# Kernel optimization log

Measured on AMD Instinct MI355X. Metric: run time of the kernel, lower is better.

## Reference

```python
import jax, jax.numpy as jnp
import numpy as np
import math

D_MODEL = 1024
N_HEADS = 16
D_K = D_MODEL // N_HEADS
B, S = 4, 2048


def setup_inputs() -> dict:
    key = jax.random.key(0)
    ks = jax.random.split(key, 11)
    sc = 1.0 / math.sqrt(D_MODEL)
    inp = {
        'q': jax.random.normal(ks[0], (B, S, D_MODEL), jnp.float32),
        'k': jax.random.normal(ks[1], (B, S, D_MODEL), jnp.float32),
        'v': jax.random.normal(ks[2], (B, S, D_MODEL), jnp.float32),
        'mask': jnp.tril(jnp.ones((S, S), jnp.int32))[None, None],  # [1,1,S,S] causal
        'wq': jax.random.normal(ks[3], (D_MODEL, D_MODEL), jnp.float32) * sc,
        'bq': jnp.zeros((D_MODEL,), jnp.float32),
        'wk': jax.random.normal(ks[4], (D_MODEL, D_MODEL), jnp.float32) * sc,
        'bk': jnp.zeros((D_MODEL,), jnp.float32),
        'wv': jax.random.normal(ks[5], (D_MODEL, D_MODEL), jnp.float32) * sc,
        'bv': jnp.zeros((D_MODEL,), jnp.float32),
        'wo': jax.random.normal(ks[6], (D_MODEL, D_MODEL), jnp.float32) * sc,
        'bo': jnp.zeros((D_MODEL,), jnp.float32),
    }
    return inp


def reference(q, k, v, mask, wq, bq, wk, bk, wv, bv, wo, bo):
    b = q.shape[0]
    # projections: [B,S,D] -> [B,H,S,d_k]
    def split_heads(x):
        return x.reshape(b, -1, N_HEADS, D_K).transpose(0, 2, 1, 3)
    qh = split_heads(q @ wq + bq)
    kh = split_heads(k @ wk + bk)
    vh = split_heads(v @ wv + bv)
    # scores: [B,H,S,S]
    scores = jnp.einsum('bhqd,bhkd->bhqk', qh, kh) / math.sqrt(D_K)
    scores = jnp.where(mask == 0, jnp.float32(-1e9), scores)
    attn = jax.nn.softmax(scores, axis=-1)
    # dropout is identity in eval mode (deterministic reference)
    ctx = jnp.einsum('bhqk,bhkd->bhqd', attn, vh)
    ctx = ctx.transpose(0, 2, 1, 3).reshape(b, -1, D_MODEL)
    return ctx @ wo + bo
```

## Files before the change

### kernel.cpp

```cpp
#include <hip/hip_runtime.h>
#include <hip/hip_bf16.h>

#define D_MODEL 1024
#define N_HEADS 16
#define DK 64
#define SEQ 2048
#define BATCH 4

typedef __attribute__((ext_vector_type(4))) float   f32v4;
typedef __attribute__((ext_vector_type(16))) float  f32v16;
typedef __attribute__((ext_vector_type(8))) __bf16  bf16x8;
typedef __attribute__((ext_vector_type(8))) unsigned short u16v8;
typedef __attribute__((ext_vector_type(4))) unsigned short u16v4;
typedef __attribute__((ext_vector_type(4))) unsigned int   u32v4;

#define QSCALE 0.18033688011112042f

__device__ __forceinline__ int swz(int byte) {
    return byte ^ (((byte >> 7) & 7) << 4);
}

__device__ __forceinline__ unsigned short bfb(float f) {
    return __builtin_bit_cast(unsigned short, (__bf16)f);
}
__device__ __forceinline__ float bff(unsigned short u) {
    return (float)__builtin_bit_cast(__bf16, u);
}

__device__ __forceinline__ f32v4 mfma16(bf16x8 a, bf16x8 b, f32v4 c) {
    return __builtin_amdgcn_mfma_f32_16x16x32_bf16(a, b, c, 0, 0, 0);
}
__device__ __forceinline__ f32v16 mfma32(bf16x8 a, bf16x8 b, f32v16 c) {
    return __builtin_amdgcn_mfma_f32_32x32x16_bf16(a, b, c, 0, 0, 0);
}

#define GL2LDS16(gp, lp) \
    __builtin_amdgcn_global_load_lds((__attribute__((address_space(1))) const void*)(gp), \
                                     (__attribute__((address_space(3))) void*)(lp), 16, 0, 0)

#define VMWAIT(N) asm volatile("s_waitcnt vmcnt(" #N ")" ::: "memory")

__global__ __launch_bounds__(256) void cvt_kernel(const float* __restrict__ src,
                                                  unsigned short* __restrict__ dst) {
    size_t e0 = ((size_t)blockIdx.x * 256 + threadIdx.x) * 8;
    f32v4 a = *(const f32v4*)(src + e0);
    f32v4 b = *(const f32v4*)(src + e0 + 4);
    u16v8 o;
#pragma unroll
    for (int j = 0; j < 4; ++j) { o[j] = bfb(a[j]); o[4 + j] = bfb(b[j]); }
    *(u16v8*)(dst + e0) = o;
}

__global__ __launch_bounds__(256) void wtrans_kernel(const float* wq, const float* wk,
                                                     const float* wv, const float* wo,
                                                     unsigned short* wt) {
    __shared__ unsigned short ts[64][65];
    int bid = blockIdx.x;
    int mat = bid >> 8;
    int tile = bid & 255;
    int kb = (tile >> 4) * 64;
    int nb = (tile & 15) * 64;
    const float* W = (mat == 0) ? wq : (mat == 1) ? wk : (mat == 2) ? wv : wo;
    unsigned short* out = wt + (size_t)mat * D_MODEL * D_MODEL;
    int t = threadIdx.x;
#pragma unroll
    for (int p = 0; p < 4; ++p) {
        int row = p * 16 + (t >> 4);
        int c0 = (t & 15) * 4;
        f32v4 v = *(const f32v4*)(W + (size_t)(kb + row) * D_MODEL + nb + c0);
#pragma unroll
        for (int j = 0; j < 4; ++j) ts[row][c0 + j] = bfb(v[j]);
    }
    __syncthreads();
#pragma unroll
    for (int p = 0; p < 2; ++p) {
        int n = p * 32 + (t >> 3);
        int k0 = (t & 7) * 8;
        u16v8 o;
#pragma unroll
        for (int j = 0; j < 8; ++j) o[j] = ts[k0 + j][n];
        *(u16v8*)(out + (size_t)(nb + n) * D_MODEL + kb + k0) = o;
    }
}

template<int OMODE>
__global__ __launch_bounds__(512, 1) void gemm2_kernel(const unsigned short* __restrict__ A,
                                                       const unsigned short* __restrict__ Wt,
                                                       const float* __restrict__ bias, void* Cptr) {
    __shared__ unsigned short lds[3][(256 + 128) * 64];
    int bid0 = blockIdx.x;
    int xcd = bid0 & 7, i = bid0 >> 3;
    int mb = (xcd * 4 + (i >> 3)) * 256;
    int nb = (i & 7) * 128;
    int tid = threadIdx.x;
    int lane = tid & 63, wid = tid >> 6;
    int l15 = lane & 15, g = lane >> 4;
    int r7 = lane >> 3, slot = lane & 7;
    int wr = wid >> 1, wc = wid & 1;
    int ssrc = (slot ^ r7) * 8;

    f32v4 acc[4][4] = {};

    char* p0 = (char*)lds[0];
    char* p1 = (char*)lds[1];
    char* p2 = (char*)lds[2];

    auto stage = [&](char* buf, int k0) {
#pragma unroll
        for (int ii = 0; ii < 4; ++ii) {
            int c = ii * 8 + wid;
            GL2LDS16(A + (size_t)(mb + c * 8 + r7) * D_MODEL + k0 + ssrc, buf + c * 1024);
        }
#pragma unroll
        for (int ii = 0; ii < 2; ++ii) {
            int c = ii * 8 + wid;
            GL2LDS16(Wt + (size_t)(nb + c * 8 + r7) * D_MODEL + k0 + ssrc, buf + 32768 + c * 1024);
        }
    };
    auto fragA = [&](char* buf, int row, int kk) -> bf16x8 {
        int sl = (kk * 4 + g) ^ (row & 7);
        return *(bf16x8*)(buf + row * 128 + sl * 16);
    };
    auto fragB = [&](char* buf, int row, int kk) -> bf16x8 {
        int sl = (kk * 4 + g) ^ (row & 7);
        return *(bf16x8*)(buf + 32768 + row * 128 + sl * 16);
    };

    stage(p0, 0);
    stage(p1, 64);
    VMWAIT(6);
    __builtin_amdgcn_s_barrier();
    __builtin_amdgcn_sched_barrier(0);

    for (int t = 0; t < 16; ++t) {
        if (t + 2 < 16) stage(p2, (t + 2) * 64);
#pragma unroll
        for (int kk = 0; kk < 2; ++kk) {
            bf16x8 fa[4], fb[4];
            if constexpr (OMODE != 2) {
#pragma unroll
                for (int mt = 0; mt < 4; ++mt) fa[mt] = fragA(p0, wr * 64 + mt * 16 + l15, kk);
#pragma unroll
                for (int nt = 0; nt < 4; ++nt) fb[nt] = fragB(p0, wc * 64 + nt * 16 + l15, kk);
            } else {
#pragma unroll
                for (int xx = 0; xx < 4; ++xx) fa[xx] = fragB(p0, wc * 64 + xx * 16 + l15, kk);
#pragma unroll
                for (int yy = 0; yy < 4; ++yy) fb[yy] = fragA(p0, wr * 64 + yy * 16 + l15, kk);
            }
            __builtin_amdgcn_s_setprio(1);
#pragma unroll
            for (int a = 0; a < 4; ++a)
#pragma unroll
                for (int b = 0; b < 4; ++b)
                    acc[a][b] = mfma16(fa[a], fb[b], acc[a][b]);
            __builtin_amdgcn_s_setprio(0);
        }
        if (t < 14) { VMWAIT(6); } else { VMWAIT(0); }
        __builtin_amdgcn_s_barrier();
        __builtin_amdgcn_sched_barrier(0);
        char* tp = p0; p0 = p1; p1 = p2; p2 = tp;
    }

    if constexpr (OMODE != 2) {
#pragma unroll
        for (int nt = 0; nt < 4; ++nt) {
            int n = nb + wc * 64 + nt * 16 + l15;
            float bv = bias[n];
#pragma unroll
            for (int mt = 0; mt < 4; ++mt) {
#pragma unroll
                for (int r = 0; r < 4; ++r) {
                    int m = mb + wr * 64 + mt * 16 + 4 * g + r;
                    float val = acc[mt][nt][r] + bv;
                    if constexpr (OMODE == 0) {
                        unsigned short* out = (unsigned short*)Cptr;
                        int bb = m >> 11, ss = m & 2047, hh = n >> 6, dd = n & 63;
                        out[(((size_t)(bb * N_HEADS + hh)) * SEQ + ss) * DK + dd] = bfb(val);
                    } else {
                        float* out = (float*)Cptr;
                        out[(size_t)m * D_MODEL + n] = val;
                    }
                }
            }
        }
    } else {
        unsigned short* out = (unsigned short*)Cptr;
#pragma unroll
        for (int xx = 0; xx < 4; ++xx) {
#pragma unroll
            for (int r = 0; r < 4; ++r) {
                int n = nb + wc * 64 + xx * 16 + 4 * g + r;
                float bv = bias[n];
                int hh = n >> 6, dd = n & 63;
#pragma unroll
                for (int yy = 0; yy < 4; ++yy) {
                    int tok = mb + wr * 64 + yy * 16 + l15;
                    int bb = tok >> 11, ss = tok & 2047;
                    float val = acc[xx][yy][r] + bv;
                    out[((size_t)(bb * N_HEADS + hh) * DK + dd) * SEQ + ss] = bfb(val);
                }
            }
        }
    }
}

__global__ __launch_bounds__(256, 4) void attn_kernel(const unsigned short* Qh, const unsigned short* Kh,
                                                      const unsigned short* Vt, unsigned short* ctxp) {
    __shared__ unsigned short k_lds[2][64 * 64];
    __shared__ unsigned short v_lds[2][64 * 64];
    int bid = blockIdx.x;
    int jq = bid >> 8, x = (bid >> 6) & 3;
    int tile = (jq == 0) ? (15 - x) : (jq == 1) ? (8 + x) : (jq == 2) ? (7 - x) : x;
    int bh = bid & 63;
    int bb = bh >> 4, hh = bh & 15;
    int tid = threadIdx.x;
    int wid = tid >> 6, lane = tid & 63;
    int l31 = lane & 31, hi = lane >> 5;
    int qw0 = tile * 128 + wid * 32;
    int qg = qw0 + l31;
    const unsigned short* Qb = Qh + (size_t)bh * SEQ * DK;
    const unsigned short* Kb = Kh + (size_t)bh * SEQ * DK;
    const unsigned short* Vb = Vt + (size_t)bh * DK * SEQ;

    bf16x8 qf[4];
#pragma unroll
    for (int ks = 0; ks < 4; ++ks) {
        u16v8 raw = *(const u16v8*)(Qb + (size_t)qg * DK + ks * 16 + hi * 8);
        u16v8 sc;
#pragma unroll
        for (int j = 0; j < 8; ++j) sc[j] = bfb(bff(raw[j]) * QSCALE);
        qf[ks] = __builtin_bit_cast(bf16x8, sc);
    }

    f32v16 o0 = {}, o1 = {};
    float mrun = -1e30f, lsum = 0.f;
    int n_kt = 2 * tile + 2;

    const int klane = 16 * (lane ^ (lane >> 3));
    const int vlane = 16 * ((lane & 7) ^ (lane >> 3));
    auto stage = [&](int bufi, int kg) {
        const char* kb0 = (const char*)(Kb + (size_t)kg * DK);
        const char* vb0 = (const char*)Vb + (size_t)kg * 2;
#pragma unroll
        for (int jj = 0; jj < 2; ++jj) {
            int base = wid * 2048 + jj * 1024;
            GL2LDS16(kb0 + base + klane, (char*)k_lds[bufi] + base);
            GL2LDS16(vb0 + (size_t)(wid * 16 + jj * 8 + (lane >> 3)) * (SEQ * 2) + vlane,
                     (char*)v_lds[bufi] + base);
        }
    };

#define PACK2(a, b) (((unsigned)bfb(b) << 16) | (unsigned)bfb(a))
#define PVSTEP(tt, r0, ks, vl)                                                          \
    {                                                                                   \
        unsigned x0 = PACK2(tt[r0 + 0], tt[r0 + 1]);                                    \
        unsigned x1 = PACK2(tt[r0 + 2], tt[r0 + 3]);                                    \
        unsigned x2 = PACK2(tt[r0 + 4], tt[r0 + 5]);                                    \
        unsigned x3 = PACK2(tt[r0 + 6], tt[r0 + 7]);                                    \
        unsigned sx0 = (unsigned)__shfl_xor((int)x0, 32);                               \
        unsigned sx1 = (unsigned)__shfl_xor((int)x1, 32);                               \
        unsigned sx2 = (unsigned)__shfl_xor((int)x2, 32);                               \
        unsigned sx3 = (unsigned)__shfl_xor((int)x3, 32);                               \
        u32v4 w;                                                                        \
        w[0] = hi ? sx2 : x0;                                                           \
        w[1] = hi ? sx3 : x1;                                                           \
        w[2] = hi ? x2 : sx0;                                                           \
        w[3] = hi ? x3 : sx1;                                                           \
        bf16x8 paf = __builtin_bit_cast(bf16x8, w);                                     \
        bf16x8 vf0 = *(bf16x8*)((char*)(vl) + swz(l31 * 128 + ks * 32 + hi * 16));      \
        bf16x8 vf1 = *(bf16x8*)((char*)(vl) + swz((32 + l31) * 128 + ks * 32 + hi * 16)); \
        o0 = mfma32(paf, vf0, o0);                                                      \
        o1 = mfma32(paf, vf1, o1);                                                      \
    }

    auto compute_tile = [&](int ktb, const unsigned short* kl, const unsigned short* vl) {
        if (ktb > qw0 + 31) return;
        f32v16 t0 = {}, t1 = {};
        __builtin_amdgcn_s_setprio(1);
#pragma unroll
        for (int ks = 0; ks < 4; ++ks) {
            bf16x8 kf0 = *(bf16x8*)((char*)kl + swz(l31 * 128 + ks * 32 + hi * 16));
            bf16x8 kf1 = *(bf16x8*)((char*)kl + swz((32 + l31) * 128 + ks * 32 + hi * 16));
            t0 = mfma32(kf0, qf[ks], t0);
            t1 = mfma32(kf1, qf[ks], t1);
        }
        __builtin_amdgcn_s_setprio(0);
        if (ktb + 63 > qw0) {
#pragma unroll
            for (int r = 0; r < 16; ++r) {
                int off = (r & 3) + 8 * (r >> 2) + 4 * hi;
                if (ktb + off > qg) t0[r] = -1e30f;
                if (ktb + 32 + off > qg) t1[r] = -1e30f;
            }
        }
        float mx = fmaxf(t0[0], t0[1]);
#pragma unroll
        for (int r = 2; r < 16; ++r) mx = fmaxf(mx, t0[r]);
#pragma unroll
        for (int r = 0; r < 16; ++r) mx = fmaxf(mx, t1[r]);
        mx = fmaxf(mx, __shfl_xor(mx, 32));
        if (__any(mx > mrun + 8.f)) {
            float mn = fmaxf(mrun, mx);
            float co = __builtin_amdgcn_exp2f(mrun - mn);
            mrun = mn;
            lsum *= co;
#pragma unroll
            for (int r = 0; r < 16; ++r) {
                int off = (r & 3) + 8 * (r >> 2) + 4 * hi;
                float cr = __shfl(co, off);
                o0[r] *= cr;
                o1[r] *= cr;
            }
        }
#pragma unroll
        for (int r = 0; r < 16; ++r) {
            t0[r] = __builtin_amdgcn_exp2f(t0[r] - mrun);
            t1[r] = __builtin_amdgcn_exp2f(t1[r] - mrun);
            lsum += t0[r] + t1[r];
        }
        __builtin_amdgcn_s_setprio(1);
        PVSTEP(t0, 0, 0, vl)
        PVSTEP(t0, 8, 1, vl)
        PVSTEP(t1, 0, 2, vl)
        PVSTEP(t1, 8, 3, vl)
        __builtin_amdgcn_s_setprio(0);
    };

    stage(0, 0);
    __syncthreads();
    int buf = 0;
    for (int kt = 0; kt < n_kt; ++kt) {
        if (kt + 1 < n_kt) stage(buf ^ 1, (kt + 1) * 64);
        compute_tile(kt * 64, k_lds[buf], v_lds[buf]);
        __syncthreads();
        buf ^= 1;
    }

    float lt = lsum + __shfl_xor(lsum, 32);
    float rinv = 1.f / lt;
#pragma unroll
    for (int r = 0; r < 16; ++r) {
        int off = (r & 3) + 8 * (r >> 2) + 4 * hi;
        float rr = __shfl(rinv, off);
        int qq = qw0 + off;
        size_t base = ((size_t)(bb * SEQ + qq)) * D_MODEL + hh * DK;
        ctxp[base + l31] = bfb(o0[r] * rr);
        ctxp[base + 32 + l31] = bfb(o1[r] * rr);
    }
#undef PVSTEP
#undef PACK2
}

extern "C" void kernel_launch(void* const* d_in, const int* in_sizes, int n_in,
                              void* d_out, int out_size, void* d_ws, size_t ws_size,
                              hipStream_t stream) {
    const float* q  = (const float*)d_in[0];
    const float* k  = (const float*)d_in[1];
    const float* v  = (const float*)d_in[2];
    const float* wq = (const float*)d_in[4];
    const float* bq = (const float*)d_in[5];
    const float* wk = (const float*)d_in[6];
    const float* bk = (const float*)d_in[7];
    const float* wv = (const float*)d_in[8];
    const float* bv = (const float*)d_in[9];
    const float* wo = (const float*)d_in[10];
    const float* bo = (const float*)d_in[11];

    unsigned short* ws  = (unsigned short*)d_ws;
    const size_t M8 = (size_t)8 * 1024 * 1024;
    unsigned short* Qh = ws;
    unsigned short* Kh = ws + M8;
    unsigned short* Vt = ws + 2 * M8;
    unsigned short* X  = ws + 3 * M8;
    unsigned short* WT = ws + 4 * M8;
    const size_t MM = (size_t)D_MODEL * D_MODEL;

    wtrans_kernel<<<dim3(1024), dim3(256), 0, stream>>>(wq, wk, wv, wo, WT);
    cvt_kernel<<<dim3(4096), dim3(256), 0, stream>>>(q, X);
    gemm2_kernel<0><<<dim3(256), dim3(512), 0, stream>>>(X, WT + 0 * MM, bq, Qh);
    cvt_kernel<<<dim3(4096), dim3(256), 0, stream>>>(k, X);
    gemm2_kernel<0><<<dim3(256), dim3(512), 0, stream>>>(X, WT + 1 * MM, bk, Kh);
    cvt_kernel<<<dim3(4096), dim3(256), 0, stream>>>(v, X);
    gemm2_kernel<2><<<dim3(256), dim3(512), 0, stream>>>(X, WT + 2 * MM, bv, Vt);
    attn_kernel<<<dim3(1024), dim3(256), 0, stream>>>(Qh, Kh, Vt, X);
    gemm2_kernel<1><<<dim3(256), dim3(512), 0, stream>>>(X, WT + 3 * MM, bo, (float*)d_out);
}
```

Baseline: 184.4 us.

## Fuse fp32-to-bf16 input conversion into projection GEMMs; use permlane32 swap in PV

Removes the three standalone cvt kernels. The Q/K/V projection GEMMs now load fp32 activations into registers, convert them to bf16 and write them into swizzled LDS, in a register-staged pipeline alongside the existing direct global-to-LDS weight loads. This avoids a bf16 round trip through HBM and three kernel launches, at the cost of extra VGPRs, VALU conversion work and an LDS wait before each barrier. Separately, the attention PV step replaces four cross-half shuffles plus selects with two v_permlane32_swap instructions.

```diff
diff --git a/kernel.cpp b/kernel.cpp
--- a/kernel.cpp
+++ b/kernel.cpp
@@ -39,17 +39,7 @@
                                      (__attribute__((address_space(3))) void*)(lp), 16, 0, 0)
 
 #define VMWAIT(N) asm volatile("s_waitcnt vmcnt(" #N ")" ::: "memory")
-
-__global__ __launch_bounds__(256) void cvt_kernel(const float* __restrict__ src,
-                                                  unsigned short* __restrict__ dst) {
-    size_t e0 = ((size_t)blockIdx.x * 256 + threadIdx.x) * 8;
-    f32v4 a = *(const f32v4*)(src + e0);
-    f32v4 b = *(const f32v4*)(src + e0 + 4);
-    u16v8 o;
-#pragma unroll
-    for (int j = 0; j < 4; ++j) { o[j] = bfb(a[j]); o[4 + j] = bfb(b[j]); }
-    *(u16v8*)(dst + e0) = o;
-}
+#define LGKM0()   asm volatile("s_waitcnt lgkmcnt(0)" ::: "memory")
 
 __global__ __launch_bounds__(256) void wtrans_kernel(const float* wq, const float* wk,
                                                      const float* wv, const float* wo,
@@ -83,15 +73,15 @@
     }
 }
 
-template<int OMODE>
-__global__ __launch_bounds__(512, 1) void gemm2_kernel(const unsigned short* __restrict__ A,
+template<int OMODE, int AF32>
+__global__ __launch_bounds__(512, 1) void gemm2_kernel(const void* __restrict__ Aptr,
                                                        const unsigned short* __restrict__ Wt,
                                                        const float* __restrict__ bias, void* Cptr) {
     __shared__ unsigned short lds[3][(256 + 128) * 64];
     int bid0 = blockIdx.x;
-    int xcd = bid0 & 7, i = bid0 >> 3;
-    int mb = (xcd * 4 + (i >> 3)) * 256;
-    int nb = (i & 7) * 128;
+    int xcd = bid0 & 7, blki = bid0 >> 3;
+    int mb = (xcd * 4 + (blki >> 3)) * 256;
+    int nb = (blki & 7) * 128;
     int tid = threadIdx.x;
     int lane = tid & 63, wid = tid >> 6;
     int l15 = lane & 15, g = lane >> 4;
@@ -105,16 +95,46 @@
     char* p1 = (char*)lds[1];
     char* p2 = (char*)lds[2];
 
-    auto stage = [&](char* buf, int k0) {
-#pragma unroll
-        for (int ii = 0; ii < 4; ++ii) {
-            int c = ii * 8 + wid;
-            GL2LDS16(A + (size_t)(mb + c * 8 + r7) * D_MODEL + k0 + ssrc, buf + c * 1024);
-        }
-#pragma unroll
-        for (int ii = 0; ii < 2; ++ii) {
-            int c = ii * 8 + wid;
-            GL2LDS16(Wt + (size_t)(nb + c * 8 + r7) * D_MODEL + k0 + ssrc, buf + 32768 + c * 1024);
+    const unsigned short* Ab = (const unsigned short*)Aptr;
+    const float*          Af = (const float*)Aptr;
+    int arow = tid >> 4;
+    int acol = (tid & 15) * 4;
+
+    f32v4 a_stg[8];
+
+    auto stage_issue = [&](char* buf, int k0) {
+        if constexpr (AF32) {
+#pragma unroll
+            for (int j = 0; j < 8; ++j)
+                a_stg[j] = *(const f32v4*)(Af + (size_t)(mb + j * 32 + arow) * D_MODEL + k0 + acol);
+#pragma unroll
+            for (int ii = 0; ii < 2; ++ii) {
+                int c = ii * 8 + wid;
+                GL2LDS16(Wt + (size_t)(nb + c * 8 + r7) * D_MODEL + k0 + ssrc, buf + 32768 + c * 1024);
+            }
+        } else {
+#pragma unroll
+            for (int ii = 0; ii < 4; ++ii) {
+                int c = ii * 8 + wid;
+                GL2LDS16(Ab + (size_t)(mb + c * 8 + r7) * D_MODEL + k0 + ssrc, buf + c * 1024);
+            }
+#pragma unroll
+            for (int ii = 0; ii < 2; ++ii) {
+                int c = ii * 8 + wid;
+                GL2LDS16(Wt + (size_t)(nb + c * 8 + r7) * D_MODEL + k0 + ssrc, buf + 32768 + c * 1024);
+            }
+        }
+    };
+    auto stage_write = [&](char* buf) {
+        if constexpr (AF32) {
+#pragma unroll
+            for (int j = 0; j < 8; ++j) {
+                u16v4 o;
+#pragma unroll
+                for (int e = 0; e < 4; ++e) o[e] = bfb(a_stg[j][e]);
+                int row = j * 32 + arow;
+                *(u16v4*)(buf + swz(row * 128 + (tid & 15) * 8)) = o;
+            }
         }
     };
     auto fragA = [&](char* buf, int row, int kk) -> bf16x8 {
@@ -126,14 +146,17 @@
         return *(bf16x8*)(buf + 32768 + row * 128 + sl * 16);
     };
 
-    stage(p0, 0);
-    stage(p1, 64);
-    VMWAIT(6);
+    stage_issue(p0, 0);
+    stage_write(p0);
+    stage_issue(p1, 64);
+    stage_write(p1);
+    if constexpr (AF32) { VMWAIT(2); } else { VMWAIT(6); }
+    LGKM0();
     __builtin_amdgcn_s_barrier();
     __builtin_amdgcn_sched_barrier(0);
 
     for (int t = 0; t < 16; ++t) {
-        if (t + 2 < 16) stage(p2, (t + 2) * 64);
+        if (t + 2 < 16) stage_issue(p2, (t + 2) * 64);
 #pragma unroll
         for (int kk = 0; kk < 2; ++kk) {
             bf16x8 fa[4], fb[4];
@@ -156,7 +179,13 @@
                     acc[a][b] = mfma16(fa[a], fb[b], acc[a][b]);
             __builtin_amdgcn_s_setprio(0);
         }
-        if (t < 14) { VMWAIT(6); } else { VMWAIT(0); }
+        if (t + 2 < 16) stage_write(p2);
+        if (t < 14) {
+            if constexpr (AF32) { VMWAIT(2); } else { VMWAIT(6); }
+        } else {
+            VMWAIT(0);
+        }
+        LGKM0();
         __builtin_amdgcn_s_barrier();
         __builtin_amdgcn_sched_barrier(0);
         char* tp = p0; p0 = p1; p1 = p2; p2 = tp;
@@ -258,15 +287,10 @@
         unsigned x1 = PACK2(tt[r0 + 2], tt[r0 + 3]);                                    \
         unsigned x2 = PACK2(tt[r0 + 4], tt[r0 + 5]);                                    \
         unsigned x3 = PACK2(tt[r0 + 6], tt[r0 + 7]);                                    \
-        unsigned sx0 = (unsigned)__shfl_xor((int)x0, 32);                               \
-        unsigned sx1 = (unsigned)__shfl_xor((int)x1, 32);                               \
-        unsigned sx2 = (unsigned)__shfl_xor((int)x2, 32);                               \
-        unsigned sx3 = (unsigned)__shfl_xor((int)x3, 32);                               \
+        asm volatile("v_permlane32_swap_b32 %0, %1" : "+v"(x0), "+v"(x2));              \
+        asm volatile("v_permlane32_swap_b32 %0, %1" : "+v"(x1), "+v"(x3));              \
         u32v4 w;                                                                        \
-        w[0] = hi ? sx2 : x0;                                                           \
-        w[1] = hi ? sx3 : x1;                                                           \
-        w[2] = hi ? x2 : sx0;                                                           \
-        w[3] = hi ? x3 : sx1;                                                           \
+        w[0] = x0;  w[1] = x1;  w[2] = x2;  w[3] = x3;                                  \
         bf16x8 paf = __builtin_bit_cast(bf16x8, w);                                     \
         bf16x8 vf0 = *(bf16x8*)((char*)(vl) + swz(l31 * 128 + ks * 32 + hi * 16));      \
         bf16x8 vf1 = *(bf16x8*)((char*)(vl) + swz((32 + l31) * 128 + ks * 32 + hi * 16)); \
@@ -377,12 +401,9 @@
     const size_t MM = (size_t)D_MODEL * D_MODEL;
 
     wtrans_kernel<<<dim3(1024), dim3(256), 0, stream>>>(wq, wk, wv, wo, WT);
-    cvt_kernel<<<dim3(4096), dim3(256), 0, stream>>>(q, X);
-    gemm2_kernel<0><<<dim3(256), dim3(512), 0, stream>>>(X, WT + 0 * MM, bq, Qh);
-    cvt_kernel<<<dim3(4096), dim3(256), 0, stream>>>(k, X);
-    gemm2_kernel<0><<<dim3(256), dim3(512), 0, stream>>>(X, WT + 1 * MM, bk, Kh);
-    cvt_kernel<<<dim3(4096), dim3(256), 0, stream>>>(v, X);
-    gemm2_kernel<2><<<dim3(256), dim3(512), 0, stream>>>(X, WT + 2 * MM, bv, Vt);
+    gemm2_kernel<0, 1><<<dim3(256), dim3(512), 0, stream>>>(q, WT + 0 * MM, bq, Qh);
+    gemm2_kernel<0, 1><<<dim3(256), dim3(512), 0, stream>>>(k, WT + 1 * MM, bk, Kh);
+    gemm2_kernel<2, 1><<<dim3(256), dim3(512), 0, stream>>>(v, WT + 2 * MM, bv, Vt);
     attn_kernel<<<dim3(1024), dim3(256), 0, stream>>>(Qh, Kh, Vt, X);
-    gemm2_kernel<1><<<dim3(256), dim3(512), 0, stream>>>(X, WT + 3 * MM, bo, (float*)d_out);
-}
+    gemm2_kernel<1, 0><<<dim3(256), dim3(512), 0, stream>>>(X, WT + 3 * MM, bo, (float*)d_out);
+}
```

Result: faster. 170.1 us (-7.7%).
